# Optimization experiments

Hardware: AMD Instinct MI355X
Metric: run time of the kernel (lower is better)

The kernel has to match this reference:

```python
import jax, jax.numpy as jnp
import numpy as np

B, N, E, F, G = 32, 512, 4, 128, 64
EMB, HID = 128, 256  # NodeEmbedding: Linear(E*G=256 -> 256) + BN + ELU + Linear(256 -> 128)
NUM_EDGES = 8192
BN_EPS = 1e-5


def setup_inputs() -> dict:
    key = jax.random.key(0)
    ks = jax.random.split(key, 8)
    X = jax.random.normal(ks[0], (B, N, F), dtype=jnp.float32)
    edges = jax.random.randint(ks[1], (B, E, 2, NUM_EDGES), 0, N, dtype=jnp.int64)
    # per-edge-type projection W_e: [F, G] (glorot)
    Ws = jax.random.normal(ks[2], (E, F, G), dtype=jnp.float32) * np.sqrt(2.0 / (F + G))
    # attention vectors a_e: [2G, 1]
    a = jax.random.normal(ks[3], (E, 2 * G, 1), dtype=jnp.float32) * (1.414 * np.sqrt(2.0 / (2 * G + 1)))
    lin0_w = jax.random.normal(ks[4], (E * G, HID), dtype=jnp.float32) * np.sqrt(2.0 / (E * G + HID))
    lin0_b = jnp.zeros((HID,), dtype=jnp.float32)
    bn_gamma = jnp.ones((HID,), dtype=jnp.float32)
    bn_beta = jnp.zeros((HID,), dtype=jnp.float32)
    lin1_w = jax.random.normal(ks[5], (HID, EMB), dtype=jnp.float32) * np.sqrt(2.0 / (HID + EMB))
    lin1_b = jnp.zeros((EMB,), dtype=jnp.float32)
    return {"X": X, "edges": edges, "Ws": Ws, "a": a, "lin0_w": lin0_w,
            "lin0_b": lin0_b, "bn_gamma": bn_gamma, "bn_beta": bn_beta,
            "lin1_w": lin1_w, "lin1_b": lin1_b}


def _dense_adj(edges):
    # COO -> dense, summing duplicates like torch.sparse_coo_tensor(...).to_dense()
    b_ix = jnp.arange(B)[:, None, None]
    e_ix = jnp.arange(E)[None, :, None]
    src = edges[:, :, 0, :]
    dst = edges[:, :, 1, :]
    A = jnp.zeros((B, E, N, N), dtype=jnp.float32)
    return A.at[b_ix, e_ix, src, dst].add(1.0)


def reference(X, edges, Ws, a, lin0_w, lin0_b, bn_gamma, bn_beta, lin1_w, lin1_b):
    A = _dense_adj(edges)                                   # [B,E,N,N]
    Wh = jnp.einsum('bnf,efg->beng', X, Ws)                 # [B,E,N,G]
    Wh1 = jnp.einsum('beng,ego->beno', Wh, a[:, :G, :])     # [B,E,N,1]
    Wh2 = jnp.einsum('beng,ego->beno', Wh, a[:, G:, :])     # [B,E,N,1]
    scores = (Wh1 + jnp.swapaxes(Wh2, 2, 3)) * A            # [B,E,N,N] (masked-to-0, NOT -inf: faithful)
    att = jax.nn.softmax(scores, axis=-1)
    H = jnp.einsum('benm,bemg->beng', att * A, Wh)          # [B,E,N,G]
    H = jnp.transpose(H, (0, 2, 1, 3)).reshape(B * N, E * G)
    # NodeEmbedding MLP (BatchNorm1d in training mode: batch stats, biased var)
    h = H @ lin0_w + lin0_b
    mu = jnp.mean(h, axis=0)
    var = jnp.mean((h - mu) ** 2, axis=0)
    h = (h - mu) * jax.lax.rsqrt(var + BN_EPS) * bn_gamma + bn_beta
    h = jax.nn.elu(h)
    out = h @ lin1_w + lin1_b
    return out.reshape(B, N, EMB)
```

## Files before the change

kernel.cpp:

```cpp
#include <hip/hip_runtime.h>

#define Bx 32
#define Nx 512
#define Ex 4
#define Fx 128
#define Gx 64
#define HIDx 256
#define EMBx 128
#define NEDGE 8192

typedef __attribute__((ext_vector_type(8))) short bf16x8;
typedef __attribute__((ext_vector_type(4))) float f32x4;

#define L2E 1.44269504f

__device__ __forceinline__ ushort f2bf(float x) {
    unsigned int u = __float_as_uint(x);
    u += 0x7fffu + ((u >> 16) & 1u);
    return (ushort)(u >> 16);
}
__device__ __forceinline__ float bf2f(ushort h) {
    return __uint_as_float(((unsigned int)h) << 16);
}

__global__ __launch_bounds__(512) void k0b(const int* __restrict__ edges,
                                           const float* __restrict__ w0,
                                           const float* __restrict__ w1f,
                                           const float* __restrict__ Wsf,
                                           ushort* __restrict__ W0T,
                                           ushort* __restrict__ W1T,
                                           ushort* __restrict__ WsT,
                                           ushort* __restrict__ binned,
                                           int* __restrict__ offs) {
    __shared__ int hist8[8][8];
    __shared__ int offl[9];
    __shared__ int cur[8];
    int blk = blockIdx.x, tid = threadIdx.x;
    if (blk < 128) {
        int wave = tid >> 6;
        if (tid < 64) ((int*)hist8)[tid] = 0;
        __syncthreads();
        const int4* s4p = (const int4*)(edges + (size_t)blk * 2 * NEDGE);
        const int4* d4p = (const int4*)(edges + (size_t)blk * 2 * NEDGE + NEDGE);
        for (int i = tid; i < NEDGE / 4; i += 512) {
            int4 s4 = s4p[i];
            atomicAdd(&hist8[wave][s4.x >> 6], 1);
            atomicAdd(&hist8[wave][s4.y >> 6], 1);
            atomicAdd(&hist8[wave][s4.z >> 6], 1);
            atomicAdd(&hist8[wave][s4.w >> 6], 1);
        }
        __syncthreads();
        if (tid == 0) {
            int run = 0;
            for (int t = 0; t < 8; ++t) {
                offl[t] = run;
                int s = 0;
                #pragma unroll
                for (int w = 0; w < 8; ++w) s += hist8[w][t];
                run += s;
            }
            offl[8] = run;
            for (int t = 0; t <= 8; ++t) offs[blk * 9 + t] = offl[t];
        }
        __syncthreads();
        if (tid < 8) cur[tid] = offl[tid];
        __syncthreads();
        ushort* bout = binned + (size_t)blk * NEDGE;
        for (int i = tid; i < NEDGE / 4; i += 512) {
            int4 s4 = s4p[i]; int4 d4 = d4p[i];
            int ss[4] = {s4.x, s4.y, s4.z, s4.w};
            int dd[4] = {d4.x, d4.y, d4.z, d4.w};
            #pragma unroll
            for (int u = 0; u < 4; ++u) {
                int t = ss[u] >> 6;
                int pos = atomicAdd(&cur[t], 1);
                bout[pos] = (ushort)(((ss[u] & 63) << 9) | dd[u]);
            }
        }
    } else if (blk < 256) {
        int idx = (blk - 128) * 512 + tid;
        int j = idx >> 8, k = idx & 255;
        W0T[j * HIDx + k] = f2bf(w0[k * HIDx + j]);
    } else if (blk < 320) {
        int idx = (blk - 256) * 512 + tid;
        int j = idx >> 8, k = idx & 255;
        W1T[j * HIDx + k] = f2bf(w1f[k * EMBx + j]);
    } else {
        int idx = (blk - 320) * 512 + tid;
        int eg = idx >> 7, f = idx & 127;
        WsT[eg * Fx + f] = f2bf(Wsf[((eg >> 6) * Fx + f) * Gx + (eg & 63)]);
    }
}

__global__ __launch_bounds__(256) void k1_wh(const float* __restrict__ X,
                                             const ushort* __restrict__ WsT,
                                             const float* __restrict__ a,
                                             ushort* __restrict__ Whb,
                                             float* __restrict__ w1,
                                             float* __restrict__ w2) {
    __shared__ ushort sXb[64 * 128];
    int id = blockIdx.x;
    int e = id & 3;
    int rest = id >> 2;
    int tile = rest & 7;
    int b = rest >> 3;
    int be = b * 4 + e;
    int n0 = tile * 64;
    int tid = threadIdx.x;
    for (int i = tid; i < 2048; i += 256) {
        int row = i >> 5, kq = i & 31;
        float4 xv = *(const float4*)&X[(size_t)(b * Nx + n0 + row) * Fx + kq * 4];
        ushort4 hv;
        hv.x = f2bf(xv.x); hv.y = f2bf(xv.y); hv.z = f2bf(xv.z); hv.w = f2bf(xv.w);
        unsigned int byteo = ((unsigned int)(row * 256 + kq * 8)) ^ (((unsigned int)(row & 7)) << 4);
        *(ushort4*)((char*)sXb + byteo) = hv;
    }
    __syncthreads();
    int wave = tid >> 6, lane = tid & 63;
    int arow = lane & 15, kg = lane >> 4;
    int row = wave * 16 + arow;
    f32x4 acc[4];
    #pragma unroll
    for (int t = 0; t < 4; ++t) acc[t] = (f32x4){0.f, 0.f, 0.f, 0.f};
    const ushort* WT = WsT + e * Gx * Fx;
    unsigned int aswz = ((unsigned int)(row & 7)) << 4;
    #pragma unroll
    for (int ks = 0; ks < 4; ++ks) {
        unsigned int abyte = ((unsigned int)(row * 256 + ks * 64 + kg * 16)) ^ aswz;
        bf16x8 af = *(const bf16x8*)((const char*)sXb + abyte);
        #pragma unroll
        for (int jt = 0; jt < 4; ++jt) {
            bf16x8 bf = *(const bf16x8*)&WT[(size_t)(jt * 16 + arow) * Fx + ks * 32 + kg * 8];
            acc[jt] = __builtin_amdgcn_mfma_f32_16x16x32_bf16(af, bf, acc[jt], 0, 0, 0);
        }
    }
    float a1v[4], a2v[4];
    #pragma unroll
    for (int jt = 0; jt < 4; ++jt) {
        a1v[jt] = a[e * 2 * Gx + jt * 16 + arow];
        a2v[jt] = a[e * 2 * Gx + Gx + jt * 16 + arow];
    }
    int m0 = n0 + wave * 16 + kg * 4;
    #pragma unroll
    for (int jt = 0; jt < 4; ++jt) {
        int g = jt * 16 + arow;
        ushort4 v;
        v.x = f2bf(acc[jt][0]); v.y = f2bf(acc[jt][1]);
        v.z = f2bf(acc[jt][2]); v.w = f2bf(acc[jt][3]);
        *(ushort4*)&Whb[((size_t)be * Gx + g) * Nx + m0] = v;
    }
    #pragma unroll
    for (int reg = 0; reg < 4; ++reg) {
        float p1 = acc[0][reg] * a1v[0] + acc[1][reg] * a1v[1] + acc[2][reg] * a1v[2] + acc[3][reg] * a1v[3];
        float p2 = acc[0][reg] * a2v[0] + acc[1][reg] * a2v[1] + acc[2][reg] * a2v[2] + acc[3][reg] * a2v[3];
        #pragma unroll
        for (int off = 1; off < 16; off <<= 1) {
            p1 += __shfl_xor(p1, off, 64);
            p2 += __shfl_xor(p2, off, 64);
        }
        if (arow == 0) {
            w1[be * Nx + m0 + reg] = p1;
            w2[be * Nx + m0 + reg] = p2;
        }
    }
}

__global__ __launch_bounds__(512) void k2_att(const ushort* __restrict__ binned,
                                              const int* __restrict__ offs,
                                              const ushort* __restrict__ Whb,
                                              const float* __restrict__ w1g,
                                              const float* __restrict__ w2g,
                                              ushort* __restrict__ Hb) {
    __shared__ ushort P[64 * 512];
    __shared__ float sw2[512];
    __shared__ float sw1[64];
    __shared__ float sinv[64];
    __shared__ float rowsum[64];
    __shared__ int   rowK[64];
    __shared__ ushort olist[4096];
    __shared__ int ocnt;
    unsigned int* cnt = (unsigned int*)P;
    int be = blockIdx.x; int b = be >> 2; int e = be & 3;
    int tile = blockIdx.y; int n0 = tile * 64;
    int tid = threadIdx.x;
    for (int i = tid; i < 64 * 132; i += 512) cnt[i] = 0u;
    sw2[tid] = w2g[be * Nx + tid] * L2E;
    if (tid < 64) {
        sw1[tid] = w1g[be * Nx + n0 + tid] * L2E;
        rowsum[tid] = 0.f; rowK[tid] = 0;
    }
    if (tid == 0) ocnt = 0;
    __syncthreads();
    int t0 = offs[be * 9 + tile], t1 = offs[be * 9 + tile + 1];
    const ushort* bin = binned + (size_t)be * NEDGE;
    for (int i = t0 + tid; i < t1; i += 512) {
        unsigned int pk = bin[i];
        unsigned int sh = (pk & 3u) * 8;
        unsigned int old = atomicAdd(&cnt[(pk >> 9) * 132 + ((pk & 511u) >> 2)], 1u << sh);
        if (((old >> sh) & 255u) == 0u) {
            int ix = atomicAdd(&ocnt, 1);
            if (ix < 4096) olist[ix] = (ushort)pk;
        }
    }
    __syncthreads();
    int tot = ocnt; if (tot > 4096) tot = 4096;
    const unsigned char* cb = (const unsigned char*)cnt;
    ushort pbv[8]; int pkv[8];
    #pragma unroll
    for (int u = 0; u < 8; ++u) {
        int i = tid + u * 512;
        bool v = i < tot;
        int pk = v ? (int)olist[i] : 0;
        int r = pk >> 9, d = pk & 511;
        float c = (float)cb[r * 528 + d];
        float ew = __builtin_exp2f(fminf((sw1[r] + sw2[d]) * c, 120.f));
        if (v) {
            atomicAdd(&rowsum[r], ew);
            atomicAdd(&rowK[r], 1);
        }
        pbv[u] = f2bf(ew * c);
        pkv[u] = v ? pk : -1;
    }
    __syncthreads();
    {
        uint4 z = {0u, 0u, 0u, 0u};
        #pragma unroll
        for (int u = 0; u < 8; ++u)
            *(uint4*)((char*)P + tid * 128 + u * 16) = z;
    }
    __syncthreads();
    #pragma unroll
    for (int u = 0; u < 8; ++u) {
        if (pkv[u] >= 0) {
            int r = pkv[u] >> 9, d = pkv[u] & 511;
            unsigned int byteo = ((unsigned int)(r * 1024 + d * 2)) ^ (((unsigned int)(r & 7)) << 4);
            *(ushort*)((char*)P + byteo) = pbv[u];
        }
    }
    if (tid < 64) sinv[tid] = 1.f / (rowsum[tid] + (float)(Nx - rowK[tid]));
    __syncthreads();
    int wave = tid >> 6, lane = tid & 63;
    int wr2 = wave >> 2, wc = wave & 3;
    int rowa = wr2 * 32 + (lane & 15);
    int rowb = rowa + 16;
    int kgrp = lane >> 4;
    f32x4 acca = {0.f, 0.f, 0.f, 0.f};
    f32x4 accb = {0.f, 0.f, 0.f, 0.f};
    const ushort* WB = Whb + (size_t)be * Gx * Nx;
    int g0 = wc * 16 + (lane & 15);
    const ushort* Bp = WB + (size_t)g0 * Nx + kgrp * 8;
    unsigned int aswza = ((unsigned int)(rowa & 7)) << 4;
    __builtin_amdgcn_s_setprio(1);
    #pragma unroll
    for (int ks = 0; ks < 16; ++ks) {
        bf16x8 bfv = *(const bf16x8*)(Bp + ks * 32);
        unsigned int ka = (unsigned int)(ks * 64 + kgrp * 16);
        unsigned int offa = ((unsigned int)(rowa * 1024) + ka) ^ aswza;
        unsigned int offb = ((unsigned int)(rowb * 1024) + ka) ^ aswza;
        bf16x8 afa = *(const bf16x8*)((const char*)P + offa);
        bf16x8 afb = *(const bf16x8*)((const char*)P + offb);
        acca = __builtin_amdgcn_mfma_f32_16x16x32_bf16(afa, bfv, acca, 0, 0, 0);
        accb = __builtin_amdgcn_mfma_f32_16x16x32_bf16(afb, bfv, accb, 0, 0, 0);
    }
    __builtin_amdgcn_s_setprio(0);
    #pragma unroll
    for (int reg = 0; reg < 4; ++reg) {
        int ra = n0 + wr2 * 32 + kgrp * 4 + reg;
        float iva = sinv[wr2 * 32 + kgrp * 4 + reg];
        float ivb = sinv[wr2 * 32 + 16 + kgrp * 4 + reg];
        Hb[((size_t)(b * Nx) + ra) * (Ex * Gx) + e * Gx + wc * 16 + (lane & 15)] =
            f2bf(acca[reg] * iva);
        Hb[((size_t)(b * Nx) + ra + 16) * (Ex * Gx) + e * Gx + wc * 16 + (lane & 15)] =
            f2bf(accb[reg] * ivb);
    }
}

__global__ __launch_bounds__(256) void k3_lin0(const ushort* __restrict__ Hb,
                                               const ushort* __restrict__ W0T,
                                               const float* __restrict__ lin0_b,
                                               ushort* __restrict__ h_pre,
                                               float* __restrict__ partials) {
    __shared__ float red_s[2][256], red_q[2][256];
    int tid = threadIdx.x, wave = tid >> 6, lane = tid & 63;
    int wr = wave >> 1, wc = wave & 1;
    int row0 = blockIdx.x * 32 + wr * 16;
    int arow = lane & 15, kg = lane >> 4;
    const ushort* A = Hb + (size_t)(row0 + arow) * HIDx;
    f32x4 acc[8];
    #pragma unroll
    for (int t = 0; t < 8; ++t) acc[t] = (f32x4){0.f, 0.f, 0.f, 0.f};
    #pragma unroll
    for (int ks = 0; ks < 8; ++ks) {
        int k0 = ks * 32 + kg * 8;
        bf16x8 af = *(const bf16x8*)&A[k0];
        #pragma unroll
        for (int jt = 0; jt < 8; ++jt) {
            bf16x8 bf = *(const bf16x8*)&W0T[(size_t)(wc * 128 + jt * 16 + arow) * HIDx + k0];
            acc[jt] = __builtin_amdgcn_mfma_f32_16x16x32_bf16(af, bf, acc[jt], 0, 0, 0);
        }
    }
    #pragma unroll
    for (int jt = 0; jt < 8; ++jt) {
        int col = wc * 128 + jt * 16 + arow;
        float b = lin0_b[col];
        float s = 0.f, q = 0.f;
        #pragma unroll
        for (int reg = 0; reg < 4; ++reg) {
            float v = acc[jt][reg] + b;
            h_pre[(size_t)(row0 + kg * 4 + reg) * HIDx + col] = f2bf(v);
            s += v; q += v * v;
        }
        s += __shfl_xor(s, 16, 64); s += __shfl_xor(s, 32, 64);
        q += __shfl_xor(q, 16, 64); q += __shfl_xor(q, 32, 64);
        if (lane < 16) { red_s[wr][col] = s; red_q[wr][col] = q; }
    }
    __syncthreads();
    int j = tid;
    partials[(size_t)blockIdx.x * 2 * HIDx + j] = red_s[0][j] + red_s[1][j];
    partials[(size_t)blockIdx.x * 2 * HIDx + HIDx + j] = red_q[0][j] + red_q[1][j];
}

__global__ __launch_bounds__(256) void k3b_stats(const float* __restrict__ partials,
                                                 const float* __restrict__ gamma,
                                                 const float* __restrict__ beta,
                                                 float* __restrict__ sb) {
    __shared__ float rs[8][32], rq[8][32];
    int jl = threadIdx.x & 31, sl = threadIdx.x >> 5;
    int j = blockIdx.x * 32 + jl;
    float s = 0.f, q = 0.f;
    for (int blk = sl; blk < 512; blk += 8) {
        s += partials[blk * 512 + j];
        q += partials[blk * 512 + 256 + j];
    }
    rs[sl][jl] = s; rq[sl][jl] = q;
    __syncthreads();
    if (threadIdx.x < 32) {
        float S = 0.f, Q = 0.f;
        #pragma unroll
        for (int t = 0; t < 8; ++t) { S += rs[t][jl]; Q += rq[t][jl]; }
        const float invM = 1.f / 16384.f;
        float mu = S * invM;
        float var = fmaxf(Q * invM - mu * mu, 0.f);
        float sc = gamma[j] * rsqrtf(var + 1e-5f);
        sb[j] = sc;
        sb[256 + j] = beta[j] - mu * sc;
    }
}

__global__ __launch_bounds__(256) void k4_lin1(const ushort* __restrict__ h_pre,
                                               const float* __restrict__ sb,
                                               const ushort* __restrict__ W1T,
                                               const float* __restrict__ lin1_b,
                                               float* __restrict__ out) {
    int tid = threadIdx.x, wave = tid >> 6, lane = tid & 63;
    int wr = wave >> 1, wc = wave & 1;
    int row0 = blockIdx.x * 32 + wr * 16;
    int arow = lane & 15, kg = lane >> 4;
    const ushort* A = h_pre + (size_t)(row0 + arow) * HIDx;
    f32x4 acc[4];
    #pragma unroll
    for (int t = 0; t < 4; ++t) acc[t] = (f32x4){0.f, 0.f, 0.f, 0.f};
    #pragma unroll
    for (int ks = 0; ks < 8; ++ks) {
        int k0 = ks * 32 + kg * 8;
        bf16x8 hv = *(const bf16x8*)&A[k0];
        float4 sc0 = *(const float4*)&sb[k0];
        float4 sc1 = *(const float4*)&sb[k0 + 4];
        float4 bi0 = *(const float4*)&sb[256 + k0];
        float4 bi1 = *(const float4*)&sb[256 + k0 + 4];
        float scv[8] = {sc0.x, sc0.y, sc0.z, sc0.w, sc1.x, sc1.y, sc1.z, sc1.w};
        float biv[8] = {bi0.x, bi0.y, bi0.z, bi0.w, bi1.x, bi1.y, bi1.z, bi1.w};
        bf16x8 af;
        #pragma unroll
        for (int u = 0; u < 8; ++u) {
            float v = bf2f((ushort)hv[u]) * scv[u] + biv[u];
            v = v > 0.f ? v : expm1f(v);
            af[u] = (short)f2bf(v);
        }
        #pragma unroll
        for (int jt = 0; jt < 4; ++jt) {
            bf16x8 bf = *(const bf16x8*)&W1T[(size_t)(wc * 64 + jt * 16 + arow) * HIDx + k0];
            acc[jt] = __builtin_amdgcn_mfma_f32_16x16x32_bf16(af, bf, acc[jt], 0, 0, 0);
        }
    }
    #pragma unroll
    for (int jt = 0; jt < 4; ++jt) {
        int col = wc * 64 + jt * 16 + arow;
        float b = lin1_b[col];
        #pragma unroll
        for (int reg = 0; reg < 4; ++reg)
            out[(size_t)(row0 + kg * 4 + reg) * EMBx + col] = acc[jt][reg] + b;
    }
}

extern "C" void kernel_launch(void* const* d_in, const int* in_sizes, int n_in,
                              void* d_out, int out_size, void* d_ws, size_t ws_size,
                              hipStream_t stream) {
    const float* X      = (const float*)d_in[0];
    const int*   edges  = (const int*)d_in[1];
    const float* Ws     = (const float*)d_in[2];
    const float* a      = (const float*)d_in[3];
    const float* lin0_w = (const float*)d_in[4];
    const float* lin0_b = (const float*)d_in[5];
    const float* gamma  = (const float*)d_in[6];
    const float* beta   = (const float*)d_in[7];
    const float* lin1_w = (const float*)d_in[8];
    const float* lin1_b = (const float*)d_in[9];
    float* ws = (float*)d_ws;

    ushort* Whb     = (ushort*)ws;
    ushort* h_pre   = (ushort*)ws;
    ushort* binned  = (ushort*)ws + 4194304;
    int*    offs    = (int*)(ws + 2621440);
    ushort* Hb      = (ushort*)(ws + 4194304);
    float*  w1      = ws + 8388608;
    float*  w2      = ws + 8454144;
    float*  partials= ws + 8519680;
    float*  sb      = ws + 8781824;
    ushort* WsT     = (ushort*)(ws + 8782336);
    ushort* W0T     = (ushort*)(ws + 8798720);
    ushort* W1T     = (ushort*)(ws + 8831488);
    float*  out     = (float*)d_out;

    k0b    <<<dim3(384), 512, 0, stream>>>(edges, lin0_w, lin1_w, Ws, W0T, W1T, WsT, binned, offs);
    k1_wh  <<<dim3(1024), 256, 0, stream>>>(X, WsT, a, Whb, w1, w2);
    k2_att <<<dim3(Bx * Ex, Nx / 64), 512, 0, stream>>>(binned, offs, Whb, w1, w2, Hb);
    k3_lin0<<<dim3(512), 256, 0, stream>>>(Hb, W0T, lin0_b, h_pre, partials);
    k3b_stats<<<8, 256, 0, stream>>>(partials, gamma, beta, sb);
    k4_lin1<<<dim3(512), 256, 0, stream>>>(h_pre, sb, W1T, lin1_b, out);
}
```

Baseline: 121.1 us.

## Merge edge binning, weight transposes and Wh projection into one launch; wave-aggregate olist appends

Combines the edge-binning/weight-transpose kernel and the Wh projection kernel into a single launch with block-index ranges, so each Wh block transposes its own Ws slice into shared memory instead of reading a pre-transposed global copy. This removes one kernel launch and the dependency between them, at the cost of redundant per-block transposition of Ws. The attention kernel's atomic append to the occupied-entry list is replaced by a wave ballot with a single leader atomic, cutting LDS atomic contention.

```diff
diff --git a/kernel.cpp b/kernel.cpp
--- a/kernel.cpp
+++ b/kernel.cpp
@@ -23,31 +23,35 @@
     return __uint_as_float(((unsigned int)h) << 16);
 }
 
-__global__ __launch_bounds__(512) void k0b(const int* __restrict__ edges,
-                                           const float* __restrict__ w0,
-                                           const float* __restrict__ w1f,
-                                           const float* __restrict__ Wsf,
-                                           ushort* __restrict__ W0T,
-                                           ushort* __restrict__ W1T,
-                                           ushort* __restrict__ WsT,
-                                           ushort* __restrict__ binned,
-                                           int* __restrict__ offs) {
-    __shared__ int hist8[8][8];
-    __shared__ int offl[9];
-    __shared__ int cur[8];
+__global__ __launch_bounds__(256) void kA(const int* __restrict__ edges,
+                                          const float* __restrict__ X,
+                                          const float* __restrict__ Wsf,
+                                          const float* __restrict__ a,
+                                          const float* __restrict__ w0f,
+                                          const float* __restrict__ w1f,
+                                          ushort* __restrict__ Whb,
+                                          float* __restrict__ w1,
+                                          float* __restrict__ w2,
+                                          ushort* __restrict__ W0T,
+                                          ushort* __restrict__ W1T,
+                                          ushort* __restrict__ binned,
+                                          int* __restrict__ offs) {
     int blk = blockIdx.x, tid = threadIdx.x;
     if (blk < 128) {
+        __shared__ int hist4[4][8];
+        __shared__ int offl[9];
+        __shared__ int cur[8];
         int wave = tid >> 6;
-        if (tid < 64) ((int*)hist8)[tid] = 0;
+        if (tid < 32) ((int*)hist4)[tid] = 0;
         __syncthreads();
         const int4* s4p = (const int4*)(edges + (size_t)blk * 2 * NEDGE);
         const int4* d4p = (const int4*)(edges + (size_t)blk * 2 * NEDGE + NEDGE);
-        for (int i = tid; i < NEDGE / 4; i += 512) {
+        for (int i = tid; i < NEDGE / 4; i += 256) {
             int4 s4 = s4p[i];
-            atomicAdd(&hist8[wave][s4.x >> 6], 1);
-            atomicAdd(&hist8[wave][s4.y >> 6], 1);
-            atomicAdd(&hist8[wave][s4.z >> 6], 1);
-            atomicAdd(&hist8[wave][s4.w >> 6], 1);
+            atomicAdd(&hist4[wave][s4.x >> 6], 1);
+            atomicAdd(&hist4[wave][s4.y >> 6], 1);
+            atomicAdd(&hist4[wave][s4.z >> 6], 1);
+            atomicAdd(&hist4[wave][s4.w >> 6], 1);
         }
         __syncthreads();
         if (tid == 0) {
@@ -56,7 +60,7 @@
                 offl[t] = run;
                 int s = 0;
                 #pragma unroll
-                for (int w = 0; w < 8; ++w) s += hist8[w][t];
+                for (int w = 0; w < 4; ++w) s += hist4[w][t];
                 run += s;
             }
             offl[8] = run;
@@ -66,7 +70,7 @@
         if (tid < 8) cur[tid] = offl[tid];
         __syncthreads();
         ushort* bout = binned + (size_t)blk * NEDGE;
-        for (int i = tid; i < NEDGE / 4; i += 512) {
+        for (int i = tid; i < NEDGE / 4; i += 256) {
             int4 s4 = s4p[i]; int4 d4 = d4p[i];
             int ss[4] = {s4.x, s4.y, s4.z, s4.w};
             int dd[4] = {d4.x, d4.y, d4.z, d4.w};
@@ -77,91 +81,82 @@
                 bout[pos] = (ushort)(((ss[u] & 63) << 9) | dd[u]);
             }
         }
-    } else if (blk < 256) {
-        int idx = (blk - 128) * 512 + tid;
-        int j = idx >> 8, k = idx & 255;
-        W0T[j * HIDx + k] = f2bf(w0[k * HIDx + j]);
-    } else if (blk < 320) {
-        int idx = (blk - 256) * 512 + tid;
-        int j = idx >> 8, k = idx & 255;
+    } else if (blk < 1152) {
+        __shared__ ushort sXb[64 * 128];
+        __shared__ ushort sWT[64 * 136];
+        int id = blk - 128;
+        int e = id & 3;
+        int rest = id >> 2;
+        int tile = rest & 7;
+        int b = rest >> 3;
+        int be = b * 4 + e;
+        int n0 = tile * 64;
+        const float* We = Wsf + e * Fx * Gx;
+        for (int i = tid; i < Gx * Fx; i += 256) {
+            int f = i & 127, g = i >> 7;
+            sWT[g * 136 + f] = f2bf(We[f * 64 + g]);
+        }
+        for (int i = tid; i < 2048; i += 256) {
+            int row = i >> 5, kq = i & 31;
+            float4 xv = *(const float4*)&X[(size_t)(b * Nx + n0 + row) * Fx + kq * 4];
+            ushort4 hv;
+            hv.x = f2bf(xv.x); hv.y = f2bf(xv.y); hv.z = f2bf(xv.z); hv.w = f2bf(xv.w);
+            unsigned int byteo = ((unsigned int)(row * 256 + kq * 8)) ^ (((unsigned int)(row & 7)) << 4);
+            *(ushort4*)((char*)sXb + byteo) = hv;
+        }
+        __syncthreads();
+        int wave = tid >> 6, lane = tid & 63;
+        int arow = lane & 15, kg = lane >> 4;
+        int row = wave * 16 + arow;
+        f32x4 acc[4];
+        #pragma unroll
+        for (int t = 0; t < 4; ++t) acc[t] = (f32x4){0.f, 0.f, 0.f, 0.f};
+        unsigned int aswz = ((unsigned int)(row & 7)) << 4;
+        #pragma unroll
+        for (int ks = 0; ks < 4; ++ks) {
+            unsigned int abyte = ((unsigned int)(row * 256 + ks * 64 + kg * 16)) ^ aswz;
+            bf16x8 af = *(const bf16x8*)((const char*)sXb + abyte);
+            #pragma unroll
+            for (int jt = 0; jt < 4; ++jt) {
+                bf16x8 bf = *(const bf16x8*)&sWT[(jt * 16 + arow) * 136 + ks * 32 + kg * 8];
+                acc[jt] = __builtin_amdgcn_mfma_f32_16x16x32_bf16(af, bf, acc[jt], 0, 0, 0);
+            }
+        }
+        float a1v[4], a2v[4];
+        #pragma unroll
+        for (int jt = 0; jt < 4; ++jt) {
+            a1v[jt] = a[e * 2 * Gx + jt * 16 + arow];
+            a2v[jt] = a[e * 2 * Gx + Gx + jt * 16 + arow];
+        }
+        int m0 = n0 + wave * 16 + kg * 4;
+        #pragma unroll
+        for (int jt = 0; jt < 4; ++jt) {
+            int g = jt * 16 + arow;
+            ushort4 v;
+            v.x = f2bf(acc[jt][0]); v.y = f2bf(acc[jt][1]);
+            v.z = f2bf(acc[jt][2]); v.w = f2bf(acc[jt][3]);
+            *(ushort4*)&Whb[((size_t)be * Gx + g) * Nx + m0] = v;
+        }
+        #pragma unroll
+        for (int reg = 0; reg < 4; ++reg) {
+            float p1 = acc[0][reg] * a1v[0] + acc[1][reg] * a1v[1] + acc[2][reg] * a1v[2] + acc[3][reg] * a1v[3];
+            float p2 = acc[0][reg] * a2v[0] + acc[1][reg] * a2v[1] + acc[2][reg] * a2v[2] + acc[3][reg] * a2v[3];
+            #pragma unroll
+            for (int off = 1; off < 16; off <<= 1) {
+                p1 += __shfl_xor(p1, off, 64);
+                p2 += __shfl_xor(p2, off, 64);
+            }
+            if (arow == 0) {
+                w1[be * Nx + m0 + reg] = p1;
+                w2[be * Nx + m0 + reg] = p2;
+            }
+        }
+    } else if (blk < 1408) {
+        int j = blk - 1152, k = tid;
+        W0T[j * HIDx + k] = f2bf(w0f[k * HIDx + j]);
+    } else {
+        int j = blk - 1408, k = tid;
         W1T[j * HIDx + k] = f2bf(w1f[k * EMBx + j]);
-    } else {
-        int idx = (blk - 320) * 512 + tid;
-        int eg = idx >> 7, f = idx & 127;
-        WsT[eg * Fx + f] = f2bf(Wsf[((eg >> 6) * Fx + f) * Gx + (eg & 63)]);
-    }
-}
-
-__global__ __launch_bounds__(256) void k1_wh(const float* __restrict__ X,
-                                             const ushort* __restrict__ WsT,
-                                             const float* __restrict__ a,
-                                             ushort* __restrict__ Whb,
-                                             float* __restrict__ w1,
-                                             float* __restrict__ w2) {
-    __shared__ ushort sXb[64 * 128];
-    int id = blockIdx.x;
-    int e = id & 3;
-    int rest = id >> 2;
-    int tile = rest & 7;
-    int b = rest >> 3;
-    int be = b * 4 + e;
-    int n0 = tile * 64;
-    int tid = threadIdx.x;
-    for (int i = tid; i < 2048; i += 256) {
-        int row = i >> 5, kq = i & 31;
-        float4 xv = *(const float4*)&X[(size_t)(b * Nx + n0 + row) * Fx + kq * 4];
-        ushort4 hv;
-        hv.x = f2bf(xv.x); hv.y = f2bf(xv.y); hv.z = f2bf(xv.z); hv.w = f2bf(xv.w);
-        unsigned int byteo = ((unsigned int)(row * 256 + kq * 8)) ^ (((unsigned int)(row & 7)) << 4);
-        *(ushort4*)((char*)sXb + byteo) = hv;
-    }
-    __syncthreads();
-    int wave = tid >> 6, lane = tid & 63;
-    int arow = lane & 15, kg = lane >> 4;
-    int row = wave * 16 + arow;
-    f32x4 acc[4];
-    #pragma unroll
-    for (int t = 0; t < 4; ++t) acc[t] = (f32x4){0.f, 0.f, 0.f, 0.f};
-    const ushort* WT = WsT + e * Gx * Fx;
-    unsigned int aswz = ((unsigned int)(row & 7)) << 4;
-    #pragma unroll
-    for (int ks = 0; ks < 4; ++ks) {
-        unsigned int abyte = ((unsigned int)(row * 256 + ks * 64 + kg * 16)) ^ aswz;
-        bf16x8 af = *(const bf16x8*)((const char*)sXb + abyte);
-        #pragma unroll
-        for (int jt = 0; jt < 4; ++jt) {
-            bf16x8 bf = *(const bf16x8*)&WT[(size_t)(jt * 16 + arow) * Fx + ks * 32 + kg * 8];
-            acc[jt] = __builtin_amdgcn_mfma_f32_16x16x32_bf16(af, bf, acc[jt], 0, 0, 0);
-        }
-    }
-    float a1v[4], a2v[4];
-    #pragma unroll
-    for (int jt = 0; jt < 4; ++jt) {
-        a1v[jt] = a[e * 2 * Gx + jt * 16 + arow];
-        a2v[jt] = a[e * 2 * Gx + Gx + jt * 16 + arow];
-    }
-    int m0 = n0 + wave * 16 + kg * 4;
-    #pragma unroll
-    for (int jt = 0; jt < 4; ++jt) {
-        int g = jt * 16 + arow;
-        ushort4 v;
-        v.x = f2bf(acc[jt][0]); v.y = f2bf(acc[jt][1]);
-        v.z = f2bf(acc[jt][2]); v.w = f2bf(acc[jt][3]);
-        *(ushort4*)&Whb[((size_t)be * Gx + g) * Nx + m0] = v;
-    }
-    #pragma unroll
-    for (int reg = 0; reg < 4; ++reg) {
-        float p1 = acc[0][reg] * a1v[0] + acc[1][reg] * a1v[1] + acc[2][reg] * a1v[2] + acc[3][reg] * a1v[3];
-        float p2 = acc[0][reg] * a2v[0] + acc[1][reg] * a2v[1] + acc[2][reg] * a2v[2] + acc[3][reg] * a2v[3];
-        #pragma unroll
-        for (int off = 1; off < 16; off <<= 1) {
-            p1 += __shfl_xor(p1, off, 64);
-            p2 += __shfl_xor(p2, off, 64);
-        }
-        if (arow == 0) {
-            w1[be * Nx + m0 + reg] = p1;
-            w2[be * Nx + m0 + reg] = p2;
-        }
     }
 }
 
@@ -193,13 +188,22 @@
     __syncthreads();
     int t0 = offs[be * 9 + tile], t1 = offs[be * 9 + tile + 1];
     const ushort* bin = binned + (size_t)be * NEDGE;
+    int lane = tid & 63;
     for (int i = t0 + tid; i < t1; i += 512) {
         unsigned int pk = bin[i];
         unsigned int sh = (pk & 3u) * 8;
         unsigned int old = atomicAdd(&cnt[(pk >> 9) * 132 + ((pk & 511u) >> 2)], 1u << sh);
-        if (((old >> sh) & 255u) == 0u) {
-            int ix = atomicAdd(&ocnt, 1);
-            if (ix < 4096) olist[ix] = (ushort)pk;
+        bool own = ((old >> sh) & 255u) == 0u;
+        unsigned long long m = __ballot(own);
+        if (m) {
+            int leader = __ffsll((long long)m) - 1;
+            int base = 0;
+            if (lane == leader) base = atomicAdd(&ocnt, __popcll(m));
+            base = __shfl(base, leader, 64);
+            if (own) {
+                int ix = base + __popcll(m & ((1ull << lane) - 1ull));
+                if (ix < 4096) olist[ix] = (ushort)pk;
+            }
         }
     }
     __syncthreads();
@@ -239,7 +243,7 @@
     }
     if (tid < 64) sinv[tid] = 1.f / (rowsum[tid] + (float)(Nx - rowK[tid]));
     __syncthreads();
-    int wave = tid >> 6, lane = tid & 63;
+    int wave = tid >> 6;
     int wr2 = wave >> 2, wc = wave & 3;
     int rowa = wr2 * 32 + (lane & 15);
     int rowb = rowa + 16;
@@ -417,13 +421,12 @@
     float*  w2      = ws + 8454144;
     float*  partials= ws + 8519680;
     float*  sb      = ws + 8781824;
-    ushort* WsT     = (ushort*)(ws + 8782336);
     ushort* W0T     = (ushort*)(ws + 8798720);
     ushort* W1T     = (ushort*)(ws + 8831488);
     float*  out     = (float*)d_out;
 
-    k0b    <<<dim3(384), 512, 0, stream>>>(edges, lin0_w, lin1_w, Ws, W0T, W1T, WsT, binned, offs);
-    k1_wh  <<<dim3(1024), 256, 0, stream>>>(X, WsT, a, Whb, w1, w2);
+    kA     <<<dim3(1536), 256, 0, stream>>>(edges, X, Ws, a, lin0_w, lin1_w,
+                                            Whb, w1, w2, W0T, W1T, binned, offs);
     k2_att <<<dim3(Bx * Ex, Nx / 64), 512, 0, stream>>>(binned, offs, Whb, w1, w2, Hb);
     k3_lin0<<<dim3(512), 256, 0, stream>>>(Hb, W0T, lin0_b, h_pre, partials);
     k3b_stats<<<8, 256, 0, stream>>>(partials, gamma, beta, sb);
```

Result: slower. 128.5 us (+6.2%).
